# Kernel tuning notes

Hardware: AMD Instinct MI355X
Metric: run time of the kernel (lower is better)

The kernel has to match this reference:

```python
import jax, jax.numpy as jnp
import numpy as np

B, T, S, G, D, H, W, CHUNK = 2, 4096, 4096, 64, 1024, 16, 512, 256
HD = D // H


def setup_inputs() -> dict:
    key = jax.random.key(0)
    ks = jax.random.split(key, 16)
    std = 1.0 / np.sqrt(D)
    w = lambda k: jax.random.normal(k, (D, D), jnp.float32) * std
    b = lambda k: jax.random.normal(k, (D,), jnp.float32) * 0.01
    return {
        "query": jax.random.normal(ks[0], (B, T, D), jnp.float32),
        "encoder_out": jax.random.normal(ks[1], (B, S, D), jnp.float32),
        "global_tokens": jax.random.normal(ks[2], (B, G, D), jnp.float32),
        "qw": w(ks[3]), "qb": b(ks[4]),
        "kw": w(ks[5]), "kb": b(ks[6]),
        "vw": w(ks[7]), "vb": b(ks[8]),
        "gkw": w(ks[9]), "gkb": b(ks[10]),
        "gvw": w(ks[11]), "gvb": b(ks[12]),
        "ow": w(ks[13]), "ob": b(ks[14]),
        "compression_ratio": 1,
    }


def reference(query, encoder_out, global_tokens, qw, qb, kw, kb, vw, vb,
              gkw, gkb, gvw, gvb, ow, ob, compression_ratio):
    scale = jnp.float32(np.sqrt(HD))
    r = jnp.float32(compression_ratio)
    # expected raw position for each decoder step, clamped to valid src range
    expected = jnp.clip((jnp.arange(T, dtype=jnp.float32) / r).astype(jnp.int32), 0, S - 1)
    expected = jnp.broadcast_to(expected[None], (B, T))  # [B,T]

    lin = lambda x, wt, bs: x @ wt.T + bs  # torch nn.Linear: y = x W^T + b
    q = lin(query, qw, qb).reshape(B, T, H, HD).transpose(0, 2, 1, 3)            # [B,H,T,HD]
    gk = lin(global_tokens, gkw, gkb).reshape(B, G, H, HD).transpose(0, 2, 1, 3)  # [B,H,G,HD]
    gv = lin(global_tokens, gvw, gvb).reshape(B, G, H, HD).transpose(0, 2, 1, 3)
    ak = lin(encoder_out, kw, kb).reshape(B, S, H, HD).transpose(0, 2, 1, 3)      # [B,H,S,HD]
    av = lin(encoder_out, vw, vb).reshape(B, S, H, HD).transpose(0, 2, 1, 3)

    nC = T // CHUNK
    # per-(batch,chunk) window start, from the middle query's expected position
    centers = expected.reshape(B, nC, CHUNK)[:, :, CHUNK // 2]   # [B,nC]
    win_start = jnp.clip(centers - W // 2, 0, S - W)             # [B,nC]; window always full length W
    idx = win_start[:, :, None] + jnp.arange(W)[None, None, :]   # [B,nC,W]

    gather = lambda kv_b, idx_b: kv_b[:, idx_b, :]               # [H,S,HD],[nC,W] -> [H,nC,W,HD]
    wk = jax.vmap(gather)(ak, idx)                               # [B,H,nC,W,HD]
    wv = jax.vmap(gather)(av, idx)

    qc = q.reshape(B, H, nC, CHUNK, HD)
    sg = jnp.einsum('bhcqd,bhgd->bhcqg', qc, gk) / scale          # global scores  [B,H,nC,CHUNK,G]
    sl = jnp.einsum('bhcqd,bhcwd->bhcqw', qc, wk) / scale         # windowed scores [B,H,nC,CHUNK,W]
    attn = jax.nn.softmax(jnp.concatenate([sg, sl], axis=-1), axis=-1)
    out = (jnp.einsum('bhcqg,bhgd->bhcqd', attn[..., :G], gv)
           + jnp.einsum('bhcqw,bhcwd->bhcqd', attn[..., G:], wv))  # [B,H,nC,CHUNK,HD]
    out = out.reshape(B, H, T, HD).transpose(0, 2, 1, 3).reshape(B, T, D)
    return lin(out, ow, ob)
```

## Files before the change

### kernel.cpp

```cpp
#include <hip/hip_runtime.h>

typedef unsigned short u16;
typedef unsigned int u32;
typedef __attribute__((ext_vector_type(4))) float f32x4;
typedef __attribute__((ext_vector_type(16))) float f32x16;
typedef __attribute__((ext_vector_type(8))) short bf16x8;

constexpr int B_ = 2, T_ = 4096, S_ = 4096, G_ = 64, D_ = 1024, H_ = 16, W_ = 512, CHUNK_ = 256;
constexpr int NC_ = T_ / CHUNK_;
constexpr int NT_ = (G_ + W_) / 32;

__device__ __forceinline__ u16 f2bf(float x) {
  u32 u = __builtin_bit_cast(u32, x);
  return (u16)((u + 0x7FFFu + ((u >> 16) & 1u)) >> 16);
}

__global__ __launch_bounds__(256) void cvt_all_kernel(const float* __restrict__ q, const float* __restrict__ e,
                                                      const float* __restrict__ g, const float* __restrict__ w0,
                                                      const float* __restrict__ w1, const float* __restrict__ w2,
                                                      const float* __restrict__ w3, const float* __restrict__ w4,
                                                      const float* __restrict__ w5, u16* __restrict__ dst) {
  int blk = blockIdx.x;
  const float* src;
  int sblk;
  if (blk < 8192) { src = q; sblk = 0; }
  else if (blk < 16384) { src = e; sblk = 8192; }
  else if (blk < 16512) { src = g; sblk = 16384; }
  else if (blk < 17536) { src = w0; sblk = 16512; }
  else if (blk < 18560) { src = w1; sblk = 17536; }
  else if (blk < 19584) { src = w2; sblk = 18560; }
  else if (blk < 20608) { src = w3; sblk = 19584; }
  else if (blk < 21632) { src = w4; sblk = 20608; }
  else { src = w5; sblk = 21632; }
  int li = (blk - sblk) * 256 + threadIdx.x;
  size_t gi = (size_t)blk * 256 + threadIdx.x;
  float4 v = ((const float4*)src)[li];
  uint2 o;
  o.x = (u32)f2bf(v.x) | ((u32)f2bf(v.y) << 16);
  o.y = (u32)f2bf(v.z) | ((u32)f2bf(v.w) << 16);
  ((uint2*)dst)[gi] = o;
}

__global__ __launch_bounds__(256, 2) void proj_kernel(const u16* __restrict__ ex, const u16* __restrict__ qx,
                                                      const u16* __restrict__ gx, const u16* __restrict__ wgt,
                                                      const float* __restrict__ qb, const float* __restrict__ kbias,
                                                      const float* __restrict__ vbias, const float* __restrict__ gkb,
                                                      const float* __restrict__ gvb, u16* __restrict__ q_bf,
                                                      u16* __restrict__ k_bf, u16* __restrict__ gk_bf) {
  __shared__ char lds[73728];
  constexpr size_t NW = (size_t)D_ * D_;
  constexpr size_t NQs = (size_t)B_ * T_ * D_;
  constexpr size_t NGs = (size_t)B_ * G_ * D_;
  const int tid = threadIdx.x;
  const int lane = tid & 63;
  const int wid = tid >> 6;
  const int wm = wid >> 1, wn = wid & 1;
  const int l15 = lane & 15, kg = lane >> 4;

  const int bid = blockIdx.x;
  const u16 *A, *Bt;
  const float *b1, *b2;
  u16* out;
  int row0, col0, mloc;
  bool scale = false, dual = false;
  size_t dsplit = 0;
  if (bid < 512) {
    row0 = (bid & 31) * 256; col0 = (bid >> 5) * 128; mloc = 256;
    A = ex; Bt = wgt + NW; b1 = kbias; b2 = vbias; out = k_bf; dsplit = NQs; dual = true;
  } else if (bid < 768) {
    int i = bid - 512;
    row0 = (i & 31) * 256; col0 = (i >> 5) * 128; mloc = 256;
    A = qx; Bt = wgt; b1 = qb; b2 = qb; out = q_bf; scale = true;
  } else {
    int i = bid - 768;
    row0 = 0; col0 = i * 128; mloc = 128;
    A = gx; Bt = wgt + 3 * NW; b1 = gkb; b2 = gvb; out = gk_bf; dsplit = NGs; dual = true;
  }
  const float* bp = b1;
  u16* op = out;
  if (dual && col0 >= 1024) { bp = b2 - 1024; op = out + (dsplit - 1024); }

  f32x4 acc[8][4];
#pragma unroll
  for (int i = 0; i < 8; i++)
#pragma unroll
    for (int j = 0; j < 4; j++)
#pragma unroll
      for (int r = 0; r < 4; r++) acc[i][j][r] = 0.f;

  const char* Abase = (const char*)A;
  const char* Bbase = (const char*)Bt;
  const int swb = 16 * ((tid & 3) ^ ((tid >> 3) & 3));

  auto stageA = [&](int slot, int kt) {
#pragma unroll
    for (int p = 0; p < 4; p++) {
      int dst = slot * 16384 + p * 4096 + tid * 16;
      const char* g = Abase + (size_t)(row0 + p * 64 + (tid >> 2)) * 2048 + kt * 64 + swb;
      __builtin_amdgcn_global_load_lds((const __attribute__((address_space(1))) void*)g,
                                       (__attribute__((address_space(3))) void*)(lds + dst), 16, 0, 0);
    }
  };
  auto stageB = [&](int slot, int kt) {
#pragma unroll
    for (int p = 0; p < 2; p++) {
      int dst = 49152 + slot * 8192 + p * 4096 + tid * 16;
      const char* g = Bbase + (size_t)(col0 + p * 64 + (tid >> 2)) * 2048 + kt * 64 + swb;
      __builtin_amdgcn_global_load_lds((const __attribute__((address_space(1))) void*)g,
                                       (__attribute__((address_space(3))) void*)(lds + dst), 16, 0, 0);
    }
  };

  stageA(0, 0); stageB(0, 0);
  stageA(1, 1); stageB(1, 1);
  asm volatile("s_waitcnt vmcnt(6)" ::: "memory");
  __builtin_amdgcn_s_barrier();

  int cur = 0, nx = 2;
  for (int t = 0; t < 32; ++t) {
    const char* Ab = lds + cur * 16384;
    const char* Bb = lds + 49152 + cur * 8192;
    bf16x8 af[4];
    bf16x8 bq[4];
#pragma unroll
    for (int ni = 0; ni < 4; ni++) {
      int r = wn * 64 + ni * 16 + l15;
      bq[ni] = *(const bf16x8*)(Bb + ((r * 64 + kg * 16) ^ (((r >> 1) & 3) << 4)));
    }
#pragma unroll
    for (int mi = 0; mi < 4; mi++) {
      int r = wm * 128 + mi * 16 + l15;
      af[mi] = *(const bf16x8*)(Ab + ((r * 64 + kg * 16) ^ (((r >> 1) & 3) << 4)));
    }
    if (t + 2 < 32) stageA(nx, t + 2);
    __builtin_amdgcn_s_barrier();
    __builtin_amdgcn_s_setprio(1);
#pragma unroll
    for (int mi = 0; mi < 4; mi++)
#pragma unroll
      for (int ni = 0; ni < 4; ni++)
        acc[mi][ni] = __builtin_amdgcn_mfma_f32_16x16x32_bf16(bq[ni], af[mi], acc[mi][ni], 0, 0, 0);
    __builtin_amdgcn_s_setprio(0);
    __builtin_amdgcn_s_barrier();
#pragma unroll
    for (int mi = 0; mi < 4; mi++) {
      int r = wm * 128 + (mi + 4) * 16 + l15;
      af[mi] = *(const bf16x8*)(Ab + ((r * 64 + kg * 16) ^ (((r >> 1) & 3) << 4)));
    }
    if (t + 2 < 32) stageB(nx, t + 2);
    __builtin_amdgcn_s_barrier();
    __builtin_amdgcn_s_setprio(1);
#pragma unroll
    for (int mi = 0; mi < 4; mi++)
#pragma unroll
      for (int ni = 0; ni < 4; ni++)
        acc[mi + 4][ni] = __builtin_amdgcn_mfma_f32_16x16x32_bf16(bq[ni], af[mi], acc[mi + 4][ni], 0, 0, 0);
    __builtin_amdgcn_s_setprio(0);
    if (t < 30) {
      asm volatile("s_waitcnt vmcnt(6)" ::: "memory");
    } else if (t == 30) {
      asm volatile("s_waitcnt vmcnt(0)" ::: "memory");
    }
    __builtin_amdgcn_s_barrier();
    cur = cur == 2 ? 0 : cur + 1;
    nx = nx == 2 ? 0 : nx + 1;
  }

  float4 bv4[4];
#pragma unroll
  for (int ni = 0; ni < 4; ni++) bv4[ni] = *(const float4*)&bp[col0 + wn * 64 + ni * 16 + kg * 4];
#pragma unroll
  for (int mi = 0; mi < 8; mi++) {
    int rloc = wm * 128 + mi * 16 + l15;
    if (rloc >= mloc) continue;
    size_t grow = (size_t)(row0 + rloc);
#pragma unroll
    for (int ni = 0; ni < 4; ni++) {
      int gcol = col0 + wn * 64 + ni * 16 + kg * 4;
      float v0 = acc[mi][ni][0] + bv4[ni].x;
      float v1 = acc[mi][ni][1] + bv4[ni].y;
      float v2 = acc[mi][ni][2] + bv4[ni].z;
      float v3 = acc[mi][ni][3] + bv4[ni].w;
      if (scale) {
        v0 *= 0.18033688011112042f; v1 *= 0.18033688011112042f;
        v2 *= 0.18033688011112042f; v3 *= 0.18033688011112042f;
      }
      uint2 o;
      asm("v_cvt_pk_bf16_f32 %0, %1, %2" : "=v"(o.x) : "v"(v0), "v"(v1));
      asm("v_cvt_pk_bf16_f32 %0, %1, %2" : "=v"(o.y) : "v"(v2), "v"(v3));
      *(uint2*)&op[grow * 1024 + gcol] = o;
    }
  }
}

__global__ __launch_bounds__(256, 2) void gemmO_kernel(const u16* __restrict__ A, const u16* __restrict__ Bt,
                                                       const float* __restrict__ bias, float* __restrict__ out) {
  __shared__ char lds[73728];
  const int tid = threadIdx.x;
  const int lane = tid & 63;
  const int wid = tid >> 6;
  const int wm = wid >> 1, wn = wid & 1;
  const int l15 = lane & 15, kg = lane >> 4;

  const int bid = blockIdx.x;
  const int row0 = (bid & 31) * 256;
  const int col0 = (bid >> 5) * 128;

  f32x4 acc[8][4];
#pragma unroll
  for (int i = 0; i < 8; i++)
#pragma unroll
    for (int j = 0; j < 4; j++)
#pragma unroll
      for (int r = 0; r < 4; r++) acc[i][j][r] = 0.f;

  const char* Abase = (const char*)A;
  const char* Bbase = (const char*)Bt;
  const int swb = 16 * ((tid & 3) ^ ((tid >> 3) & 3));

  auto stageA = [&](int slot, int kt) {
#pragma unroll
    for (int p = 0; p < 4; p++) {
      int dst = slot * 16384 + p * 4096 + tid * 16;
      const char* g = Abase + (size_t)(row0 + p * 64 + (tid >> 2)) * 2048 + kt * 64 + swb;
      __builtin_amdgcn_global_load_lds((const __attribute__((address_space(1))) void*)g,
                                       (__attribute__((address_space(3))) void*)(lds + dst), 16, 0, 0);
    }
  };
  auto stageB = [&](int slot, int kt) {
#pragma unroll
    for (int p = 0; p < 2; p++) {
      int dst = 49152 + slot * 8192 + p * 4096 + tid * 16;
      const char* g = Bbase + (size_t)(col0 + p * 64 + (tid >> 2)) * 2048 + kt * 64 + swb;
      __builtin_amdgcn_global_load_lds((const __attribute__((address_space(1))) void*)g,
                                       (__attribute__((address_space(3))) void*)(lds + dst), 16, 0, 0);
    }
  };

  stageA(0, 0); stageB(0, 0);
  stageA(1, 1); stageB(1, 1);
  asm volatile("s_waitcnt vmcnt(6)" ::: "memory");
  __builtin_amdgcn_s_barrier();

  int cur = 0, nx = 2;
  for (int t = 0; t < 32; ++t) {
    const char* Ab = lds + cur * 16384;
    const char* Bb = lds + 49152 + cur * 8192;
    bf16x8 af[4];
    bf16x8 bq[4];
#pragma unroll
    for (int ni = 0; ni < 4; ni++) {
      int r = wn * 64 + ni * 16 + l15;
      bq[ni] = *(const bf16x8*)(Bb + ((r * 64 + kg * 16) ^ (((r >> 1) & 3) << 4)));
    }
#pragma unroll
    for (int mi = 0; mi < 4; mi++) {
      int r = wm * 128 + mi * 16 + l15;
      af[mi] = *(const bf16x8*)(Ab + ((r * 64 + kg * 16) ^ (((r >> 1) & 3) << 4)));
    }
    if (t + 2 < 32) stageA(nx, t + 2);
    __builtin_amdgcn_s_barrier();
    __builtin_amdgcn_s_setprio(1);
#pragma unroll
    for (int mi = 0; mi < 4; mi++)
#pragma unroll
      for (int ni = 0; ni < 4; ni++)
        acc[mi][ni] = __builtin_amdgcn_mfma_f32_16x16x32_bf16(bq[ni], af[mi], acc[mi][ni], 0, 0, 0);
    __builtin_amdgcn_s_setprio(0);
    __builtin_amdgcn_s_barrier();
#pragma unroll
    for (int mi = 0; mi < 4; mi++) {
      int r = wm * 128 + (mi + 4) * 16 + l15;
      af[mi] = *(const bf16x8*)(Ab + ((r * 64 + kg * 16) ^ (((r >> 1) & 3) << 4)));
    }
    if (t + 2 < 32) stageB(nx, t + 2);
    __builtin_amdgcn_s_barrier();
    __builtin_amdgcn_s_setprio(1);
#pragma unroll
    for (int mi = 0; mi < 4; mi++)
#pragma unroll
      for (int ni = 0; ni < 4; ni++)
        acc[mi + 4][ni] = __builtin_amdgcn_mfma_f32_16x16x32_bf16(bq[ni], af[mi], acc[mi + 4][ni], 0, 0, 0);
    __builtin_amdgcn_s_setprio(0);
    if (t < 30) {
      asm volatile("s_waitcnt vmcnt(6)" ::: "memory");
    } else if (t == 30) {
      asm volatile("s_waitcnt vmcnt(0)" ::: "memory");
    }
    __builtin_amdgcn_s_barrier();
    cur = cur == 2 ? 0 : cur + 1;
    nx = nx == 2 ? 0 : nx + 1;
  }

  float4 bv4[4];
#pragma unroll
  for (int ni = 0; ni < 4; ni++) bv4[ni] = *(const float4*)&bias[col0 + wn * 64 + ni * 16 + kg * 4];
#pragma unroll
  for (int mi = 0; mi < 8; mi++) {
    size_t grow = (size_t)(row0 + wm * 128 + mi * 16 + l15);
#pragma unroll
    for (int ni = 0; ni < 4; ni++) {
      int gcol = col0 + wn * 64 + ni * 16 + kg * 4;
      float4 fo;
      fo.x = acc[mi][ni][0] + bv4[ni].x;
      fo.y = acc[mi][ni][1] + bv4[ni].y;
      fo.z = acc[mi][ni][2] + bv4[ni].z;
      fo.w = acc[mi][ni][3] + bv4[ni].w;
      *(float4*)&out[grow * 1024 + gcol] = fo;
    }
  }
}

__global__ __launch_bounds__(512, 4) void attn_kernel(const u16* __restrict__ q_bf, const u16* __restrict__ k_bf,
                                                      const u16* __restrict__ v_bf, const u16* __restrict__ gk_bf,
                                                      const u16* __restrict__ gv_bf, u16* __restrict__ ao,
                                                      const int* __restrict__ rptr) {
  __shared__ u16 smem[16384];
  const int c = blockIdx.x, h = blockIdx.y, b = blockIdx.z;
  const int tid = threadIdx.x;
  const int lane = tid & 63, wv = tid >> 6;
  const int l31 = lane & 31, half = lane >> 5;
  const int t0 = c * CHUNK_;

  int rr = rptr[0];
  int centert = c * CHUNK_ + CHUNK_ / 2;
  int expected = (int)((float)centert / (float)rr);
  expected = min(max(expected, 0), S_ - 1);
  int ws0 = min(max(expected - W_ / 2, 0), S_ - W_);

  bf16x8 qf[4];
  {
    const u16* qrow = q_bf + ((size_t)(b * T_ + t0 + wv * 32 + l31)) * D_ + h * 64 + half * 8;
#pragma unroll
    for (int s = 0; s < 4; s++) qf[s] = *(const bf16x8*)(qrow + s * 16);
  }

  const int skey = (tid & 255) >> 3, shq = tid & 7;
  const bool isK = tid < 256;

  auto load_tile = [&](int j) -> uint4 {
    const u16* base;
    size_t row;
    if (j < 2) {
      base = isK ? gk_bf : gv_bf;
      row = (size_t)(b * G_ + j * 32 + skey);
    } else {
      base = isK ? k_bf : v_bf;
      row = (size_t)(b * S_ + ws0 + (j - 2) * 32 + skey);
    }
    return *(const uint4*)(base + row * D_ + h * 64 + shq * 8);
  };

  f32x16 oacc[2];
#pragma unroll
  for (int i = 0; i < 2; i++)
#pragma unroll
    for (int r = 0; r < 16; r++) oacc[i][r] = 0.f;
  float mrun = -1e30f, lsum = 0.f;

  uint4 stg = load_tile(0);

  for (int j = 0; j < NT_; j++) {
    const int bsel = j & 1;
    if (isK) {
      *(uint4*)((char*)smem + bsel * 4096 + ((skey * 128 + shq * 16) ^ ((skey & 7) << 4))) = stg;
    } else {
      const u16* pv = (const u16*)&stg;
      char* bp = (char*)smem + 8192 + bsel * 5248 + shq * 656 + skey * 2;
#pragma unroll
      for (int e = 0; e < 8; e++) *(u16*)(bp + e * 80) = pv[e];
    }
    if (j + 1 < NT_) stg = load_tile(j + 1);
    __syncthreads();

    const int kbase = bsel * 4096;
    const int vtb = 8192 + bsel * 5248;

    f32x16 sacc;
#pragma unroll
    for (int r = 0; r < 16; r++) sacc[r] = 0.f;
    __builtin_amdgcn_s_setprio(1);
#pragma unroll
    for (int s = 0; s < 4; s++) {
      int kbx = kbase + ((l31 * 128 + half * 16 + s * 32) ^ ((l31 & 7) << 4));
      bf16x8 kf = *(const bf16x8*)((char*)smem + kbx);
      sacc = __builtin_amdgcn_mfma_f32_32x32x16_bf16(kf, qf[s], sacc, 0, 0, 0);
    }
    __builtin_amdgcn_s_setprio(0);

    float t0m = fmaxf(fmaxf(sacc[0], sacc[1]), sacc[2]);
    float t1m = fmaxf(fmaxf(sacc[3], sacc[4]), sacc[5]);
    float t2m = fmaxf(fmaxf(sacc[6], sacc[7]), sacc[8]);
    float t3m = fmaxf(fmaxf(sacc[9], sacc[10]), sacc[11]);
    float t4m = fmaxf(fmaxf(sacc[12], sacc[13]), sacc[14]);
    float tmax = fmaxf(fmaxf(fmaxf(t0m, t1m), fmaxf(t2m, t3m)), fmaxf(t4m, sacc[15]));
    tmax = fmaxf(tmax, __shfl_xor(tmax, 32));
    if (__any(tmax > mrun + 8.f)) {
      float mnew = fmaxf(mrun, tmax);
      float fac = __builtin_amdgcn_exp2f(mrun - mnew);
      mrun = mnew;
      lsum *= fac;
#pragma unroll
      for (int i = 0; i < 2; i++)
#pragma unroll
        for (int r = 0; r < 16; r++) oacc[i][r] *= fac;
    }
    float p[16];
#pragma unroll
    for (int r = 0; r < 16; r++) p[r] = __builtin_amdgcn_exp2f(sacc[r] - mrun);
    float s0s = (p[0] + p[1]) + (p[2] + p[3]);
    float s1s = (p[4] + p[5]) + (p[6] + p[7]);
    float s2s = (p[8] + p[9]) + (p[10] + p[11]);
    float s3s = (p[12] + p[13]) + (p[14] + p[15]);
    float tsum = (s0s + s1s) + (s2s + s3s);
    tsum += __shfl_xor(tsum, 32);
    lsum += tsum;

    u32 xs[8], px[8];
#pragma unroll
    for (int i = 0; i < 8; i++)
      asm("v_cvt_pk_bf16_f32 %0, %1, %2" : "=v"(xs[i]) : "v"(p[2 * i]), "v"(p[2 * i + 1]));
#pragma unroll
    for (int i = 0; i < 8; i++) px[i] = (u32)__shfl_xor((int)xs[i], 32);
    u32 Bk[2][4];
    Bk[0][0] = half ? px[2] : xs[0];
    Bk[0][1] = half ? px[3] : xs[1];
    Bk[0][2] = half ? xs[2] : px[0];
    Bk[0][3] = half ? xs[3] : px[1];
    Bk[1][0] = half ? px[6] : xs[4];
    Bk[1][1] = half ? px[7] : xs[5];
    Bk[1][2] = half ? xs[6] : px[4];
    Bk[1][3] = half ? xs[7] : px[5];

    int vro = vtb + l31 * 80 + ((l31 >> 3) << 4) + half * 16;
    __builtin_amdgcn_s_setprio(1);
#pragma unroll
    for (int hdf = 0; hdf < 2; hdf++) {
#pragma unroll
      for (int ks = 0; ks < 2; ks++) {
        bf16x8 vf = *(const bf16x8*)((const char*)smem + vro + hdf * 2624 + ks * 32);
        uint4 u4;
        u4.x = Bk[ks][0]; u4.y = Bk[ks][1]; u4.z = Bk[ks][2]; u4.w = Bk[ks][3];
        bf16x8 pb = __builtin_bit_cast(bf16x8, u4);
        oacc[hdf] = __builtin_amdgcn_mfma_f32_32x32x16_bf16(vf, pb, oacc[hdf], 0, 0, 0);
      }
    }
    __builtin_amdgcn_s_setprio(0);
  }

  __syncthreads();
  float inv = 1.f / lsum;
#pragma unroll
  for (int hdf = 0; hdf < 2; hdf++) {
#pragma unroll
    for (int a = 0; a < 4; a++) {
      float f0 = oacc[hdf][4 * a] * inv, f1 = oacc[hdf][4 * a + 1] * inv;
      float f2 = oacc[hdf][4 * a + 2] * inv, f3 = oacc[hdf][4 * a + 3] * inv;
      uint2 o;
      asm("v_cvt_pk_bf16_f32 %0, %1, %2" : "=v"(o.x) : "v"(f0), "v"(f1));
      asm("v_cvt_pk_bf16_f32 %0, %1, %2" : "=v"(o.y) : "v"(f2), "v"(f3));
      int off = wv * 4096 + l31 * 128 + ((16 * a + 8 * half + 64 * hdf) ^ ((l31 & 7) << 4));
      *(uint2*)((char*)smem + off) = o;
    }
  }
  __syncthreads();
#pragma unroll
  for (int it = 0; it < 4; it++) {
    int byteo = (tid + it * 512) * 16;
    int row = byteo >> 7;
    int colb = byteo & 127;
    uint4 vv = *(const uint4*)((const char*)smem + row * 128 + (colb ^ ((row & 7) << 4)));
    *(uint4*)(ao + ((size_t)(b * T_ + t0 + row)) * D_ + h * 64 + (colb >> 1)) = vv;
  }
}

extern "C" void kernel_launch(void* const* d_in, const int* in_sizes, int n_in,
                              void* d_out, int out_size, void* d_ws, size_t ws_size,
                              hipStream_t stream) {
  (void)in_sizes; (void)n_in; (void)out_size; (void)ws_size;
  const float* query = (const float*)d_in[0];
  const float* enc = (const float*)d_in[1];
  const float* glob = (const float*)d_in[2];
  const float* qw = (const float*)d_in[3];
  const float* qb = (const float*)d_in[4];
  const float* kw = (const float*)d_in[5];
  const float* kb = (const float*)d_in[6];
  const float* vw = (const float*)d_in[7];
  const float* vb = (const float*)d_in[8];
  const float* gkw = (const float*)d_in[9];
  const float* gkb = (const float*)d_in[10];
  const float* gvw = (const float*)d_in[11];
  const float* gvb = (const float*)d_in[12];
  const float* ow = (const float*)d_in[13];
  const float* ob = (const float*)d_in[14];
  const int* rp = (const int*)d_in[15];

  const size_t NQ = (size_t)B_ * T_ * D_;
  const size_t NG = (size_t)B_ * G_ * D_;
  const size_t NW = (size_t)D_ * D_;

  u16* ws = (u16*)d_ws;
  u16* qx = ws;
  u16* ex = qx + NQ;
  u16* gx = ex + NQ;
  u16* wgt = gx + NG;
  u16* q_bf = wgt + 6 * NW;
  u16* k_bf = q_bf + NQ;
  u16* v_bf = k_bf + NQ;
  u16* gk_bf = v_bf + NQ;
  u16* gv_bf = gk_bf + NG;
  u16* ao = gv_bf + NG;

  cvt_all_kernel<<<22656, 256, 0, stream>>>(query, enc, glob, qw, kw, vw, gkw, gvw, ow, ws);

  proj_kernel<<<784, 256, 0, stream>>>(ex, qx, gx, wgt, qb, kb, vb, gkb, gvb, q_bf, k_bf, gk_bf);

  attn_kernel<<<dim3(NC_, H_, B_), 512, 0, stream>>>(q_bf, k_bf, v_bf, gk_bf, gv_bf, ao, rp);

  gemmO_kernel<<<256, 256, 0, stream>>>(ao, wgt + 5 * NW, ob, (float*)d_out);
}
```

Baseline: 151.8 us.

## Split projection and output GEMM tiles across eight waves with simplified pipeline

The projection and output-projection GEMM kernels now launch 512 threads instead of 256. Each wave computes a 64x64 sub-tile instead of 128x64, which halves the accumulator registers per wave and puts more waves on the same 256x128 block tile. The main loop is restructured to issue the A and B prefetches for stage t+2 at the top of each iteration and run a single MFMA phase, dropping two intra-iteration barriers; the vmcnt waits are adjusted to match the new per-thread load count. This aims for better latency hiding and less synchronisation, at the cost of more LDS fragment reads per MFMA and possibly lower register-level reuse.

Measured after the change: 151.2 us, median of 2. No clear change (-0.4%).

```diff
diff --git a/kernel.cpp b/kernel.cpp
--- a/kernel.cpp
+++ b/kernel.cpp
@@ -41,7 +41,7 @@
   ((uint2*)dst)[gi] = o;
 }
 
-__global__ __launch_bounds__(256, 2) void proj_kernel(const u16* __restrict__ ex, const u16* __restrict__ qx,
+__global__ __launch_bounds__(512, 2) void proj_kernel(const u16* __restrict__ ex, const u16* __restrict__ qx,
                                                       const u16* __restrict__ gx, const u16* __restrict__ wgt,
                                                       const float* __restrict__ qb, const float* __restrict__ kbias,
                                                       const float* __restrict__ vbias, const float* __restrict__ gkb,
@@ -80,9 +80,9 @@
   u16* op = out;
   if (dual && col0 >= 1024) { bp = b2 - 1024; op = out + (dsplit - 1024); }
 
-  f32x4 acc[8][4];
-#pragma unroll
-  for (int i = 0; i < 8; i++)
+  f32x4 acc[4][4];
+#pragma unroll
+  for (int i = 0; i < 4; i++)
 #pragma unroll
     for (int j = 0; j < 4; j++)
 #pragma unroll
@@ -94,34 +94,31 @@
 
   auto stageA = [&](int slot, int kt) {
 #pragma unroll
-    for (int p = 0; p < 4; p++) {
-      int dst = slot * 16384 + p * 4096 + tid * 16;
-      const char* g = Abase + (size_t)(row0 + p * 64 + (tid >> 2)) * 2048 + kt * 64 + swb;
+    for (int p = 0; p < 2; p++) {
+      int dst = slot * 16384 + p * 8192 + tid * 16;
+      const char* g = Abase + (size_t)(row0 + p * 128 + (tid >> 2)) * 2048 + kt * 64 + swb;
       __builtin_amdgcn_global_load_lds((const __attribute__((address_space(1))) void*)g,
                                        (__attribute__((address_space(3))) void*)(lds + dst), 16, 0, 0);
     }
   };
   auto stageB = [&](int slot, int kt) {
-#pragma unroll
-    for (int p = 0; p < 2; p++) {
-      int dst = 49152 + slot * 8192 + p * 4096 + tid * 16;
-      const char* g = Bbase + (size_t)(col0 + p * 64 + (tid >> 2)) * 2048 + kt * 64 + swb;
-      __builtin_amdgcn_global_load_lds((const __attribute__((address_space(1))) void*)g,
-                                       (__attribute__((address_space(3))) void*)(lds + dst), 16, 0, 0);
-    }
+    int dst = 49152 + slot * 8192 + tid * 16;
+    const char* g = Bbase + (size_t)(col0 + (tid >> 2)) * 2048 + kt * 64 + swb;
+    __builtin_amdgcn_global_load_lds((const __attribute__((address_space(1))) void*)g,
+                                     (__attribute__((address_space(3))) void*)(lds + dst), 16, 0, 0);
   };
 
   stageA(0, 0); stageB(0, 0);
   stageA(1, 1); stageB(1, 1);
-  asm volatile("s_waitcnt vmcnt(6)" ::: "memory");
+  asm volatile("s_waitcnt vmcnt(3)" ::: "memory");
   __builtin_amdgcn_s_barrier();
 
   int cur = 0, nx = 2;
   for (int t = 0; t < 32; ++t) {
     const char* Ab = lds + cur * 16384;
     const char* Bb = lds + 49152 + cur * 8192;
-    bf16x8 af[4];
-    bf16x8 bq[4];
+    if (t + 2 < 32) { stageA(nx, t + 2); stageB(nx, t + 2); }
+    bf16x8 bq[4], af[4];
 #pragma unroll
     for (int ni = 0; ni < 4; ni++) {
       int r = wn * 64 + ni * 16 + l15;
@@ -129,11 +126,9 @@
     }
 #pragma unroll
     for (int mi = 0; mi < 4; mi++) {
-      int r = wm * 128 + mi * 16 + l15;
+      int r = wm * 64 + mi * 16 + l15;
       af[mi] = *(const bf16x8*)(Ab + ((r * 64 + kg * 16) ^ (((r >> 1) & 3) << 4)));
     }
-    if (t + 2 < 32) stageA(nx, t + 2);
-    __builtin_amdgcn_s_barrier();
     __builtin_amdgcn_s_setprio(1);
 #pragma unroll
     for (int mi = 0; mi < 4; mi++)
@@ -141,23 +136,8 @@
       for (int ni = 0; ni < 4; ni++)
         acc[mi][ni] = __builtin_amdgcn_mfma_f32_16x16x32_bf16(bq[ni], af[mi], acc[mi][ni], 0, 0, 0);
     __builtin_amdgcn_s_setprio(0);
-    __builtin_amdgcn_s_barrier();
-#pragma unroll
-    for (int mi = 0; mi < 4; mi++) {
-      int r = wm * 128 + (mi + 4) * 16 + l15;
-      af[mi] = *(const bf16x8*)(Ab + ((r * 64 + kg * 16) ^ (((r >> 1) & 3) << 4)));
-    }
-    if (t + 2 < 32) stageB(nx, t + 2);
-    __builtin_amdgcn_s_barrier();
-    __builtin_amdgcn_s_setprio(1);
-#pragma unroll
-    for (int mi = 0; mi < 4; mi++)
-#pragma unroll
-      for (int ni = 0; ni < 4; ni++)
-        acc[mi + 4][ni] = __builtin_amdgcn_mfma_f32_16x16x32_bf16(bq[ni], af[mi], acc[mi + 4][ni], 0, 0, 0);
-    __builtin_amdgcn_s_setprio(0);
     if (t < 30) {
-      asm volatile("s_waitcnt vmcnt(6)" ::: "memory");
+      asm volatile("s_waitcnt vmcnt(3)" ::: "memory");
     } else if (t == 30) {
       asm volatile("s_waitcnt vmcnt(0)" ::: "memory");
     }
@@ -170,8 +150,8 @@
 #pragma unroll
   for (int ni = 0; ni < 4; ni++) bv4[ni] = *(const float4*)&bp[col0 + wn * 64 + ni * 16 + kg * 4];
 #pragma unroll
-  for (int mi = 0; mi < 8; mi++) {
-    int rloc = wm * 128 + mi * 16 + l15;
+  for (int mi = 0; mi < 4; mi++) {
+    int rloc = wm * 64 + mi * 16 + l15;
     if (rloc >= mloc) continue;
     size_t grow = (size_t)(row0 + rloc);
 #pragma unroll
@@ -193,7 +173,7 @@
   }
 }
 
-__global__ __launch_bounds__(256, 2) void gemmO_kernel(const u16* __restrict__ A, const u16* __restrict__ Bt,
+__global__ __launch_bounds__(512, 2) void gemmO_kernel(const u16* __restrict__ A, const u16* __restrict__ Bt,
                                                        const float* __restrict__ bias, float* __restrict__ out) {
   __shared__ char lds[73728];
   const int tid = threadIdx.x;
@@ -206,9 +186,9 @@
   const int row0 = (bid & 31) * 256;
   const int col0 = (bid >> 5) * 128;
 
-  f32x4 acc[8][4];
-#pragma unroll
-  for (int i = 0; i < 8; i++)
+  f32x4 acc[4][4];
+#pragma unroll
+  for (int i = 0; i < 4; i++)
 #pragma unroll
     for (int j = 0; j < 4; j++)
 #pragma unroll
@@ -220,34 +200,31 @@
 
   auto stageA = [&](int slot, int kt) {
 #pragma unroll
-    for (int p = 0; p < 4; p++) {
-      int dst = slot * 16384 + p * 4096 + tid * 16;
-      const char* g = Abase + (size_t)(row0 + p * 64 + (tid >> 2)) * 2048 + kt * 64 + swb;
+    for (int p = 0; p < 2; p++) {
+      int dst = slot * 16384 + p * 8192 + tid * 16;
+      const char* g = Abase + (size_t)(row0 + p * 128 + (tid >> 2)) * 2048 + kt * 64 + swb;
       __builtin_amdgcn_global_load_lds((const __attribute__((address_space(1))) void*)g,
                                        (__attribute__((address_space(3))) void*)(lds + dst), 16, 0, 0);
     }
   };
   auto stageB = [&](int slot, int kt) {
-#pragma unroll
-    for (int p = 0; p < 2; p++) {
-      int dst = 49152 + slot * 8192 + p * 4096 + tid * 16;
-      const char* g = Bbase + (size_t)(col0 + p * 64 + (tid >> 2)) * 2048 + kt * 64 + swb;
-      __builtin_amdgcn_global_load_lds((const __attribute__((address_space(1))) void*)g,
-                                       (__attribute__((address_space(3))) void*)(lds + dst), 16, 0, 0);
-    }
+    int dst = 49152 + slot * 8192 + tid * 16;
+    const char* g = Bbase + (size_t)(col0 + (tid >> 2)) * 2048 + kt * 64 + swb;
+    __builtin_amdgcn_global_load_lds((const __attribute__((address_space(1))) void*)g,
+                                     (__attribute__((address_space(3))) void*)(lds + dst), 16, 0, 0);
   };
 
   stageA(0, 0); stageB(0, 0);
   stageA(1, 1); stageB(1, 1);
-  asm volatile("s_waitcnt vmcnt(6)" ::: "memory");
+  asm volatile("s_waitcnt vmcnt(3)" ::: "memory");
   __builtin_amdgcn_s_barrier();
 
   int cur = 0, nx = 2;
   for (int t = 0; t < 32; ++t) {
     const char* Ab = lds + cur * 16384;
     const char* Bb = lds + 49152 + cur * 8192;
-    bf16x8 af[4];
-    bf16x8 bq[4];
+    if (t + 2 < 32) { stageA(nx, t + 2); stageB(nx, t + 2); }
+    bf16x8 bq[4], af[4];
 #pragma unroll
     for (int ni = 0; ni < 4; ni++) {
       int r = wn * 64 + ni * 16 + l15;
@@ -255,11 +232,9 @@
     }
 #pragma unroll
     for (int mi = 0; mi < 4; mi++) {
-      int r = wm * 128 + mi * 16 + l15;
+      int r = wm * 64 + mi * 16 + l15;
       af[mi] = *(const bf16x8*)(Ab + ((r * 64 + kg * 16) ^ (((r >> 1) & 3) << 4)));
     }
-    if (t + 2 < 32) stageA(nx, t + 2);
-    __builtin_amdgcn_s_barrier();
     __builtin_amdgcn_s_setprio(1);
 #pragma unroll
     for (int mi = 0; mi < 4; mi++)
@@ -267,23 +242,8 @@
       for (int ni = 0; ni < 4; ni++)
         acc[mi][ni] = __builtin_amdgcn_mfma_f32_16x16x32_bf16(bq[ni], af[mi], acc[mi][ni], 0, 0, 0);
     __builtin_amdgcn_s_setprio(0);
-    __builtin_amdgcn_s_barrier();
-#pragma unroll
-    for (int mi = 0; mi < 4; mi++) {
-      int r = wm * 128 + (mi + 4) * 16 + l15;
-      af[mi] = *(const bf16x8*)(Ab + ((r * 64 + kg * 16) ^ (((r >> 1) & 3) << 4)));
-    }
-    if (t + 2 < 32) stageB(nx, t + 2);
-    __builtin_amdgcn_s_barrier();
-    __builtin_amdgcn_s_setprio(1);
-#pragma unroll
-    for (int mi = 0; mi < 4; mi++)
-#pragma unroll
-      for (int ni = 0; ni < 4; ni++)
-        acc[mi + 4][ni] = __builtin_amdgcn_mfma_f32_16x16x32_bf16(bq[ni], af[mi], acc[mi + 4][ni], 0, 0, 0);
-    __builtin_amdgcn_s_setprio(0);
     if (t < 30) {
-      asm volatile("s_waitcnt vmcnt(6)" ::: "memory");
+      asm volatile("s_waitcnt vmcnt(3)" ::: "memory");
     } else if (t == 30) {
       asm volatile("s_waitcnt vmcnt(0)" ::: "memory");
     }
@@ -296,8 +256,8 @@
 #pragma unroll
   for (int ni = 0; ni < 4; ni++) bv4[ni] = *(const float4*)&bias[col0 + wn * 64 + ni * 16 + kg * 4];
 #pragma unroll
-  for (int mi = 0; mi < 8; mi++) {
-    size_t grow = (size_t)(row0 + wm * 128 + mi * 16 + l15);
+  for (int mi = 0; mi < 4; mi++) {
+    size_t grow = (size_t)(row0 + wm * 64 + mi * 16 + l15);
 #pragma unroll
     for (int ni = 0; ni < 4; ni++) {
       int gcol = col0 + wn * 64 + ni * 16 + kg * 4;
@@ -513,9 +473,9 @@
 
   cvt_all_kernel<<<22656, 256, 0, stream>>>(query, enc, glob, qw, kw, vw, gkw, gvw, ow, ws);
 
-  proj_kernel<<<784, 256, 0, stream>>>(ex, qx, gx, wgt, qb, kb, vb, gkb, gvb, q_bf, k_bf, gk_bf);
+  proj_kernel<<<784, 512, 0, stream>>>(ex, qx, gx, wgt, qb, kb, vb, gkb, gvb, q_bf, k_bf, gk_bf);
 
   attn_kernel<<<dim3(NC_, H_, B_), 512, 0, stream>>>(q_bf, k_bf, v_bf, gk_bf, gv_bf, ao, rp);
 
-  gemmO_kernel<<<256, 256, 0, stream>>>(ao, wgt + 5 * NW, ob, (float*)d_out);
-}
+  gemmO_kernel<<<256, 512, 0, stream>>>(ao, wgt + 5 * NW, ob, (float*)d_out);
+}
```
